# Performance work log

Measured on AMD Instinct MI355X. Metric: run time of the kernel, lower is better.

Reference implementation:

```python
import jax, jax.numpy as jnp
import numpy as np

HEAD_SIZE = 64

def setup_inputs() -> dict:
    key = jax.random.key(0)
    k1, k2, k3 = jax.random.split(key, 3)
    B, T, C = 4, 4096, 1024
    x = jax.random.normal(k1, (B, T, C), dtype=jnp.float32)
    # nn.Linear(C, head_size, bias=False); stored as [in, out] so x @ W matches x @ weight.T
    Wk = jax.random.normal(k2, (C, HEAD_SIZE), dtype=jnp.float32) * (C ** -0.5)
    Wv = jax.random.normal(k3, (C, HEAD_SIZE), dtype=jnp.float32) * (C ** -0.5)
    return {"x": x, "Wk": Wk, "Wv": Wv}

def reference(x, Wk, Wv):
    # Faithful to source: q = self.key(x)  (query projection is unused -> Q == K)
    B, T, C = x.shape
    k = jnp.einsum('btc,ch->bth', x, Wk)           # [B,T,H]
    q = jnp.einsum('btc,ch->bth', x, Wk)           # same projection (source bug)
    scores = jnp.einsum('bth,bsh->bts', q, k) * (HEAD_SIZE ** -0.5)  # [B,T,T]
    causal = jnp.tril(jnp.ones((T, T), dtype=bool))
    scores = jnp.where(causal, scores, -jnp.inf)
    weights = jax.nn.softmax(scores, axis=-1)      # dropout p=0 (eval) -> identity
    v = jnp.einsum('btc,ch->bth', x, Wv)
    out = jnp.einsum('bts,bsh->bth', weights, v)   # [B,T,H]
    return out
```

## Files before the change

### kernel.cpp

```cpp
#include <hip/hip_runtime.h>

typedef short bf16x8 __attribute__((ext_vector_type(8)));
typedef float f32x4 __attribute__((ext_vector_type(4)));
typedef float f32x16 __attribute__((ext_vector_type(16)));
typedef unsigned u32x4v __attribute__((ext_vector_type(4)));

#define T_SEQ 4096
#define CDIM  1024
#define HD    64
#define NROWS 16384

__device__ inline float exp2fast(float x) {
  return __builtin_amdgcn_exp2f(x);
}

__device__ inline unsigned short f2bf(float f) {
  unsigned u = __builtin_bit_cast(unsigned, f);
  u = (u + 0x7fffu + ((u >> 16) & 1u)) >> 16;
  return (unsigned short)u;
}
__device__ inline unsigned cvt_pk_bf16(float lo, float hi) {
  unsigned r;
  asm("v_cvt_pk_bf16_f32 %0, %1, %2" : "=v"(r) : "v"(lo), "v"(hi));
  return r;
}
__device__ inline float bf2f(unsigned short u) {
  unsigned v = (unsigned)u << 16;
  return __builtin_bit_cast(float, v);
}
__device__ inline void gload_lds16(const unsigned short* g, unsigned char* l) {
  __builtin_amdgcn_global_load_lds(
      (const __attribute__((address_space(1))) unsigned int*)(const void*)g,
      (__attribute__((address_space(3))) unsigned int*)(void*)l, 16, 0, 0);
}

__global__ __launch_bounds__(256) void prep_w(
    const float* __restrict__ Wk, const float* __restrict__ Wv,
    unsigned short* __restrict__ Wt) {
  __shared__ float tile[64][68];
  const int t = threadIdx.x;
  const int mat = blockIdx.x & 1;
  const int k0 = (blockIdx.x >> 1) * 64;
  const float* W = mat ? Wv : Wk;
  #pragma unroll
  for (int pp = 0; pp < 4; ++pp) {
    int idx = t + 256 * pp, row = idx >> 4, c4 = idx & 15;
    float4 v = *(const float4*)&W[(size_t)(k0 + row) * HD + c4 * 4];
    *(float4*)&tile[row][c4 * 4] = v;
  }
  __syncthreads();
  #pragma unroll
  for (int j = 0; j < 2; ++j) {
    int n = t & 63, j8 = (t >> 6) + 4 * j;
    unsigned ow[4];
    #pragma unroll
    for (int w = 0; w < 4; ++w)
      ow[w] = cvt_pk_bf16(tile[j8 * 8 + 2 * w][n], tile[j8 * 8 + 2 * w + 1][n]);
    u32x4v ov = {ow[0], ow[1], ow[2], ow[3]};
    *(u32x4v*)&Wt[(size_t)(mat * 64 + n) * CDIM + k0 + j8 * 8] = ov;
  }
}

__global__ __launch_bounds__(256) void proj_mfma(
    const float* __restrict__ x, const unsigned short* __restrict__ Wt,
    unsigned short* __restrict__ Kb, unsigned short* __restrict__ Vb) {
  __shared__ __align__(16) unsigned char xsb[16384];
  __shared__ __align__(16) unsigned char wsb[65536];
  const int tid = threadIdx.x;
  const int lane = tid & 63, wave = tid >> 6;
  const int wm = wave & 1, wn = wave >> 1;
  const int lg = lane >> 4, lc = lane & 15;
  const int row0 = blockIdx.x * 64;

  float4 xreg[8];
  auto load_x = [&](int kk) {
    #pragma unroll
    for (int p = 0; p < 8; ++p) {
      int idx = tid + 256 * p, r = idx >> 5, c4 = idx & 31;
      xreg[p] = *(const float4*)&x[(size_t)(row0 + r) * CDIM + kk + c4 * 4];
    }
  };
  auto write_x = [&]() {
    #pragma unroll
    for (int p = 0; p < 8; ++p) {
      int idx = tid + 256 * p, r = idx >> 5, c4 = idx & 31;
      uint2 v;
      v.x = cvt_pk_bf16(xreg[p].x, xreg[p].y);
      v.y = cvt_pk_bf16(xreg[p].z, xreg[p].w);
      int byt = (r * 256 + c4 * 8) ^ ((r & 7) << 4);
      *(uint2*)(xsb + byt) = v;
    }
  };
  auto gload_W = [&](int kk, int buf) {
    unsigned char* wb = wsb + buf * 32768;
    #pragma unroll
    for (int p = 0; p < 8; ++p) {
      int ci = p * 256 + tid;
      int r = ci >> 4;
      int c8 = (ci & 15) ^ (r & 7);
      gload_lds16(&Wt[(size_t)r * CDIM + kk + c8 * 8],
                  wb + (p * 256 + wave * 64) * 16);
    }
  };

  f32x4 acc[2][4];
  #pragma unroll
  for (int mf = 0; mf < 2; ++mf)
    #pragma unroll
    for (int nf = 0; nf < 4; ++nf) acc[mf][nf] = (f32x4){0.f, 0.f, 0.f, 0.f};

  gload_W(0, 0);
  load_x(0);
  for (int kk = 0; kk < CDIM; kk += 128) {
    const int cur = (kk >> 7) & 1;
    __syncthreads();
    write_x();
    __syncthreads();
    if (kk + 128 < CDIM) { gload_W(kk + 128, cur ^ 1); load_x(kk + 128); }
    const unsigned char* wb = wsb + cur * 32768;
    #pragma unroll
    for (int dd = 0; dd < 4; ++dd) {
      bf16x8 a[2], bfr[4];
      #pragma unroll
      for (int mf = 0; mf < 2; ++mf) {
        int r = wm * 32 + mf * 16 + lc;
        int sw = (r & 7) << 4;
        a[mf] = *(const bf16x8*)(xsb + ((r * 256 + dd * 64 + lg * 16) ^ sw));
      }
      #pragma unroll
      for (int nf = 0; nf < 4; ++nf) {
        int r = wn * 64 + nf * 16 + lc;
        int sw = (r & 7) << 4;
        bfr[nf] = *(const bf16x8*)(wb + ((r * 256 + dd * 64 + lg * 16) ^ sw));
      }
      __builtin_amdgcn_s_setprio(1);
      #pragma unroll
      for (int mf = 0; mf < 2; ++mf)
        #pragma unroll
        for (int nf = 0; nf < 4; ++nf)
          acc[mf][nf] = __builtin_amdgcn_mfma_f32_16x16x32_bf16(a[mf], bfr[nf], acc[mf][nf], 0, 0, 0);
      __builtin_amdgcn_s_setprio(0);
    }
  }

  unsigned short* Ob = (wn == 0) ? Kb : Vb;
  #pragma unroll
  for (int mf = 0; mf < 2; ++mf)
    #pragma unroll
    for (int r = 0; r < 4; ++r) {
      int rg = row0 + wm * 32 + mf * 16 + lg * 4 + r;
      #pragma unroll
      for (int nf = 0; nf < 4; ++nf)
        Ob[(size_t)rg * HD + nf * 16 + lc] = f2bf(acc[mf][nf][r]);
    }
}

__global__ __launch_bounds__(256) void attn_part(
    const unsigned short* __restrict__ Kb, const unsigned short* __restrict__ Vb,
    unsigned short* __restrict__ Opart, float* __restrict__ Ml) {
  __shared__ __align__(16) unsigned char lds[32768];

  const int tid = threadIdx.x;
  const int lane = tid & 63;
  const int wq = tid >> 6;
  const int hi = lane >> 5;
  const int lq = lane & 31;

  const int b = blockIdx.x & 3;
  int qb = 0, c = 0;
  {
    int u = blockIdx.x >> 2, acc = 0;
    for (int q = 31; q >= 0; --q) {
      int nch = (q + 2) >> 1;
      if (u < acc + nch) { qb = q; c = u - acc; break; }
      acc += nch;
    }
  }
  const int kstart = c * 256;
  const int kend = min(kstart + 256, (qb + 1) * 128);
  const int nit = (kend - kstart) >> 6;
  const int q0g = qb * 128 + wq * 32;
  const int qg = q0g + lq;
  const size_t base = (size_t)b * T_SEQ;
  const float SCALE2 = 0.18033688011112042f;

  bf16x8 qf[4];
  {
    const unsigned short* qp = &Kb[(base + q0g + lq) * HD];
    #pragma unroll
    for (int dd = 0; dd < 4; ++dd) {
      bf16x8 t = *(const bf16x8*)&qp[dd * 16 + hi * 8];
      const unsigned short* ts = (const unsigned short*)&t;
      unsigned ow[4];
      #pragma unroll
      for (int w = 0; w < 4; ++w)
        ow[w] = cvt_pk_bf16(bf2f(ts[2 * w]) * SCALE2, bf2f(ts[2 * w + 1]) * SCALE2);
      u32x4v ov = {ow[0], ow[1], ow[2], ow[3]};
      qf[dd] = __builtin_bit_cast(bf16x8, ov);
    }
  }

  f32x16 oT0, oT1;
  #pragma unroll
  for (int r = 0; r < 16; ++r) { oT0[r] = 0.f; oT1[r] = 0.f; }
  float mreg = -1e30f, lreg = 0.f;

  uint4 vreg0, vreg1;
  auto gload_K = [&](int jj, int buf) {
    const size_t kv0 = (base + kstart + (size_t)jj * 64) * HD;
    unsigned char* kb = lds + buf * 16384;
    #pragma unroll
    for (int p = 0; p < 2; ++p) {
      int ci = p * 256 + tid;
      int r = ci >> 3;
      int c8 = (ci & 7) ^ (r & 7);
      gload_lds16(&Kb[kv0 + (size_t)r * HD + c8 * 8],
                  kb + (p * 256 + (tid >> 6) * 64) * 16);
    }
  };
  auto load_v = [&](int jj) {
    const size_t kv0 = (base + kstart + (size_t)jj * 64) * HD;
    int key0 = (tid & 31) * 2, d0 = (tid >> 5) * 8;
    vreg0 = *(const uint4*)&Vb[kv0 + (size_t)key0 * HD + d0];
    vreg1 = *(const uint4*)&Vb[kv0 + (size_t)(key0 + 1) * HD + d0];
  };
  auto write_v = [&](int buf) {
    unsigned char* vb = lds + buf * 16384 + 8192;
    int key0 = (tid & 31) * 2, d0 = (tid >> 5) * 8;
    const unsigned short* pa = (const unsigned short*)&vreg0;
    const unsigned short* pb = (const unsigned short*)&vreg1;
    #pragma unroll
    for (int j = 0; j < 8; ++j) {
      unsigned val = (unsigned)pa[j] | ((unsigned)pb[j] << 16);
      int d = d0 + j;
      int byt = (d * 128 + key0 * 2) ^ ((d & 7) << 4);
      *(unsigned*)(vb + byt) = val;
    }
  };

  auto qk = [&](int buf, int ksub) -> f32x16 {
    const unsigned char* kb = lds + buf * 16384;
    f32x16 sacc;
    #pragma unroll
    for (int r = 0; r < 16; ++r) sacc[r] = 0.f;
    const int krow = ksub * 32 + lq;
    const int ksw = (krow & 7) << 4;
    #pragma unroll
    for (int dd = 0; dd < 4; ++dd) {
      bf16x8 kf = *(const bf16x8*)(kb + ((krow * 128 + dd * 32 + hi * 16) ^ ksw));
      sacc = __builtin_amdgcn_mfma_f32_32x32x16_bf16(kf, qf[dd], sacc, 0, 0, 0);
    }
    return sacc;
  };
  auto maskdiag = [&](f32x16& s, int kbase_s) {
    #pragma unroll
    for (int r = 0; r < 16; ++r) {
      int key = kbase_s + (r & 3) + 8 * (r >> 2) + 4 * hi;
      if (key > qg) s[r] = -1e38f;
    }
  };
  auto max16 = [&](const f32x16& s) -> float {
    return fmaxf(
        fmaxf(fmaxf(fmaxf(s[0], s[1]), fmaxf(s[2], s[3])),
              fmaxf(fmaxf(s[4], s[5]), fmaxf(s[6], s[7]))),
        fmaxf(fmaxf(fmaxf(s[8], s[9]), fmaxf(s[10], s[11])),
              fmaxf(fmaxf(s[12], s[13]), fmaxf(s[14], s[15]))));
  };
  auto pack2 = [&](const f32x16& s, bf16x8& p1, bf16x8& p2) {
    unsigned pk[8];
    #pragma unroll
    for (int i = 0; i < 8; ++i) pk[i] = cvt_pk_bf16(s[2 * i], s[2 * i + 1]);
    unsigned wA[4], wB[4];
    #pragma unroll
    for (int i = 0; i < 2; ++i) {
      unsigned a0 = pk[i], b0 = pk[2 + i];
      unsigned sa = (unsigned)__shfl_xor((int)a0, 32);
      unsigned sb = (unsigned)__shfl_xor((int)b0, 32);
      wA[i] = hi ? sb : a0;
      wA[2 + i] = hi ? b0 : sa;
      unsigned c0 = pk[4 + i], d0v = pk[6 + i];
      unsigned sc = (unsigned)__shfl_xor((int)c0, 32);
      unsigned sd = (unsigned)__shfl_xor((int)d0v, 32);
      wB[i] = hi ? sd : c0;
      wB[2 + i] = hi ? d0v : sc;
    }
    u32x4v t1v = {wA[0], wA[1], wA[2], wA[3]};
    u32x4v t2v = {wB[0], wB[1], wB[2], wB[3]};
    p1 = __builtin_bit_cast(bf16x8, t1v);
    p2 = __builtin_bit_cast(bf16x8, t2v);
  };
  auto pv = [&](int buf, int ksub, bf16x8 pb1, bf16x8 pb2) {
    const unsigned char* vb = lds + buf * 16384 + 8192;
    const int cb = ksub * 64;
    {
      int drow = lq;
      int swz = (drow & 7) << 4;
      bf16x8 v0 = *(const bf16x8*)(vb + ((drow * 128 + cb + hi * 16) ^ swz));
      bf16x8 v1 = *(const bf16x8*)(vb + ((drow * 128 + cb + 32 + hi * 16) ^ swz));
      oT0 = __builtin_amdgcn_mfma_f32_32x32x16_bf16(v0, pb1, oT0, 0, 0, 0);
      oT0 = __builtin_amdgcn_mfma_f32_32x32x16_bf16(v1, pb2, oT0, 0, 0, 0);
    }
    {
      int drow = 32 + lq;
      int swz = (drow & 7) << 4;
      bf16x8 v0 = *(const bf16x8*)(vb + ((drow * 128 + cb + hi * 16) ^ swz));
      bf16x8 v1 = *(const bf16x8*)(vb + ((drow * 128 + cb + 32 + hi * 16) ^ swz));
      oT1 = __builtin_amdgcn_mfma_f32_32x32x16_bf16(v0, pb1, oT1, 0, 0, 0);
      oT1 = __builtin_amdgcn_mfma_f32_32x32x16_bf16(v1, pb2, oT1, 0, 0, 0);
    }
  };

  gload_K(0, 0);
  load_v(0);
  write_v(0);
  for (int jj = 0; jj < nit; ++jj) {
    const int cur = jj & 1;
    __syncthreads();
    if (jj + 1 < nit) { gload_K(jj + 1, cur ^ 1); load_v(jj + 1); }
    const int kb0 = kstart + jj * 64;

    if (kb0 + 32 <= q0g) {
      __builtin_amdgcn_s_setprio(1);
      f32x16 s0 = qk(cur, 0);
      f32x16 s1 = qk(cur, 1);
      __builtin_amdgcn_s_setprio(0);
      if (kb0 + 32 == q0g) maskdiag(s1, kb0 + 32);
      float mx = fmaxf(max16(s0), max16(s1));
      mx = fmaxf(mx, __shfl_xor(mx, 32));
      if (!__all(mx <= mreg + 11.5f)) {
        float mn = fmaxf(mreg, mx);
        float al = exp2fast(mreg - mn);
        lreg *= al;
        #pragma unroll
        for (int r = 0; r < 16; ++r) { oT0[r] *= al; oT1[r] *= al; }
        mreg = mn;
      }
      float ps = 0.f;
      #pragma unroll
      for (int r = 0; r < 16; ++r) {
        float p0 = exp2fast(s0[r] - mreg);
        float p1 = exp2fast(s1[r] - mreg);
        ps += p0 + p1;
        s0[r] = p0;
        s1[r] = p1;
      }
      lreg += ps + __shfl_xor(ps, 32);
      bf16x8 pa1, pa2, pbb1, pbb2;
      pack2(s0, pa1, pa2);
      pack2(s1, pbb1, pbb2);
      __builtin_amdgcn_s_setprio(1);
      pv(cur, 0, pa1, pa2);
      pv(cur, 1, pbb1, pbb2);
      __builtin_amdgcn_s_setprio(0);
    } else if (kb0 <= q0g) {
      __builtin_amdgcn_s_setprio(1);
      f32x16 s0 = qk(cur, 0);
      __builtin_amdgcn_s_setprio(0);
      if (kb0 == q0g) maskdiag(s0, kb0);
      float mx = max16(s0);
      mx = fmaxf(mx, __shfl_xor(mx, 32));
      if (!__all(mx <= mreg + 11.5f)) {
        float mn = fmaxf(mreg, mx);
        float al = exp2fast(mreg - mn);
        lreg *= al;
        #pragma unroll
        for (int r = 0; r < 16; ++r) { oT0[r] *= al; oT1[r] *= al; }
        mreg = mn;
      }
      float ps = 0.f;
      #pragma unroll
      for (int r = 0; r < 16; ++r) {
        float p = exp2fast(s0[r] - mreg);
        ps += p;
        s0[r] = p;
      }
      lreg += ps + __shfl_xor(ps, 32);
      bf16x8 pa1, pa2;
      pack2(s0, pa1, pa2);
      __builtin_amdgcn_s_setprio(1);
      pv(cur, 0, pa1, pa2);
      __builtin_amdgcn_s_setprio(0);
    }

    if (jj + 1 < nit) write_v(cur ^ 1);
  }

  unsigned short* op = Opart + (size_t)blockIdx.x * 8192;
  const float invl = 1.0f / lreg;
  const int qrow = wq * 32 + lq;
  #pragma unroll
  for (int g = 0; g < 4; ++g) {
    int d0 = 8 * g + 4 * hi;
    uint2 w0, w1;
    w0.x = cvt_pk_bf16(oT0[4 * g] * invl, oT0[4 * g + 1] * invl);
    w0.y = cvt_pk_bf16(oT0[4 * g + 2] * invl, oT0[4 * g + 3] * invl);
    w1.x = cvt_pk_bf16(oT1[4 * g] * invl, oT1[4 * g + 1] * invl);
    w1.y = cvt_pk_bf16(oT1[4 * g + 2] * invl, oT1[4 * g + 3] * invl);
    *(uint2*)&op[qrow * 64 + d0] = w0;
    *(uint2*)&op[qrow * 64 + d0 + 32] = w1;
  }
  if (hi == 0) {
    Ml[(size_t)blockIdx.x * 256 + qrow * 2] = mreg;
    Ml[(size_t)blockIdx.x * 256 + qrow * 2 + 1] = lreg;
  }
}

__global__ __launch_bounds__(256) void attn_merge(
    const unsigned short* __restrict__ Opart, const float* __restrict__ Ml,
    float* __restrict__ out) {
  int g = blockIdx.x * 256 + threadIdx.x;
  int d8 = (g & 7) * 8;
  int q128 = (g >> 3) & 127;
  int qb = (g >> 10) & 31;
  int b = (g >> 15) & 3;
  int nch = (qb + 2) >> 1;
  int us = 0;
  for (int q = 31; q > qb; --q) us += (q + 2) >> 1;
  float M = -1e30f;
  for (int cc = 0; cc < nch; ++cc) {
    int part = (us + cc) * 4 + b;
    M = fmaxf(M, Ml[(size_t)part * 256 + q128 * 2]);
  }
  float L = 0.f;
  float o[8];
  #pragma unroll
  for (int j = 0; j < 8; ++j) o[j] = 0.f;
  for (int cc = 0; cc < nch; ++cc) {
    int part = (us + cc) * 4 + b;
    float mc = Ml[(size_t)part * 256 + q128 * 2];
    float lc = Ml[(size_t)part * 256 + q128 * 2 + 1];
    float w = exp2fast(mc - M) * lc;
    L += w;
    uint4 v = *(const uint4*)&Opart[(size_t)part * 8192 + q128 * 64 + d8];
    const unsigned short* pv = (const unsigned short*)&v;
    #pragma unroll
    for (int j = 0; j < 8; ++j) o[j] += w * bf2f(pv[j]);
  }
  float inv = 1.0f / L;
  size_t og = ((size_t)b * T_SEQ + qb * 128 + q128) * 64 + d8;
  float4 r0 = make_float4(o[0] * inv, o[1] * inv, o[2] * inv, o[3] * inv);
  float4 r1 = make_float4(o[4] * inv, o[5] * inv, o[6] * inv, o[7] * inv);
  *(float4*)&out[og] = r0;
  *(float4*)&out[og + 4] = r1;
}

extern "C" void kernel_launch(void* const* d_in, const int* in_sizes, int n_in,
                              void* d_out, int out_size, void* d_ws, size_t ws_size,
                              hipStream_t stream) {
  const float* x  = (const float*)d_in[0];
  const float* Wk = (const float*)d_in[1];
  const float* Wv = (const float*)d_in[2];
  unsigned short* Kb = (unsigned short*)d_ws;
  unsigned short* Vb = Kb + (size_t)NROWS * HD;
  unsigned short* Wt = Vb + (size_t)NROWS * HD;
  unsigned short* Opart = Wt + (size_t)128 * CDIM;
  float* Ml = (float*)(Opart + (size_t)1088 * 8192);
  float* o = (float*)d_out;

  prep_w<<<32, 256, 0, stream>>>(Wk, Wv, Wt);
  proj_mfma<<<256, 256, 0, stream>>>(x, Wt, Kb, Vb);
  attn_part<<<1088, 256, 0, stream>>>(Kb, Vb, Opart, Ml);
  attn_merge<<<512, 256, 0, stream>>>(Opart, Ml, o);
}
```

Before: 73.67 us.

## Enlarge attention query tile to 256 rows with 512-thread blocks

The partial-attention kernel now gives each block 256 query rows split across 8 waves (512 threads) instead of 128 rows across 4 waves. Each 256-key chunk always runs 4 iterations, so each K/V tile staged in LDS is reused by twice as many query rows. This halves the number of partial blocks and merge inputs. The trade-off is more waves sharing each barrier and fewer blocks for load balancing. Only half the threads load V, and diagonal chunks now do fully masked iterations for some waves.

```diff
diff --git a/kernel.cpp b/kernel.cpp
--- a/kernel.cpp
+++ b/kernel.cpp
@@ -155,7 +155,7 @@
     }
 }
 
-__global__ __launch_bounds__(256) void attn_part(
+__global__ __launch_bounds__(512) void attn_part(
     const unsigned short* __restrict__ Kb, const unsigned short* __restrict__ Vb,
     unsigned short* __restrict__ Opart, float* __restrict__ Ml) {
   __shared__ __align__(16) unsigned char lds[32768];
@@ -170,16 +170,14 @@
   int qb = 0, c = 0;
   {
     int u = blockIdx.x >> 2, acc = 0;
-    for (int q = 31; q >= 0; --q) {
-      int nch = (q + 2) >> 1;
+    for (int q = 15; q >= 0; --q) {
+      int nch = q + 1;
       if (u < acc + nch) { qb = q; c = u - acc; break; }
       acc += nch;
     }
   }
   const int kstart = c * 256;
-  const int kend = min(kstart + 256, (qb + 1) * 128);
-  const int nit = (kend - kstart) >> 6;
-  const int q0g = qb * 128 + wq * 32;
+  const int q0g = qb * 256 + wq * 32;
   const int qg = q0g + lq;
   const size_t base = (size_t)b * T_SEQ;
   const float SCALE2 = 0.18033688011112042f;
@@ -209,32 +207,31 @@
   auto gload_K = [&](int jj, int buf) {
     const size_t kv0 = (base + kstart + (size_t)jj * 64) * HD;
     unsigned char* kb = lds + buf * 16384;
-    #pragma unroll
-    for (int p = 0; p < 2; ++p) {
-      int ci = p * 256 + tid;
-      int r = ci >> 3;
-      int c8 = (ci & 7) ^ (r & 7);
-      gload_lds16(&Kb[kv0 + (size_t)r * HD + c8 * 8],
-                  kb + (p * 256 + (tid >> 6) * 64) * 16);
-    }
+    int r = tid >> 3;
+    int c8 = (tid & 7) ^ (r & 7);
+    gload_lds16(&Kb[kv0 + (size_t)r * HD + c8 * 8], kb + (tid >> 6) * 1024);
   };
   auto load_v = [&](int jj) {
-    const size_t kv0 = (base + kstart + (size_t)jj * 64) * HD;
-    int key0 = (tid & 31) * 2, d0 = (tid >> 5) * 8;
-    vreg0 = *(const uint4*)&Vb[kv0 + (size_t)key0 * HD + d0];
-    vreg1 = *(const uint4*)&Vb[kv0 + (size_t)(key0 + 1) * HD + d0];
+    if (tid < 256) {
+      const size_t kv0 = (base + kstart + (size_t)jj * 64) * HD;
+      int key0 = (tid & 31) * 2, d0 = (tid >> 5) * 8;
+      vreg0 = *(const uint4*)&Vb[kv0 + (size_t)key0 * HD + d0];
+      vreg1 = *(const uint4*)&Vb[kv0 + (size_t)(key0 + 1) * HD + d0];
+    }
   };
   auto write_v = [&](int buf) {
-    unsigned char* vb = lds + buf * 16384 + 8192;
-    int key0 = (tid & 31) * 2, d0 = (tid >> 5) * 8;
-    const unsigned short* pa = (const unsigned short*)&vreg0;
-    const unsigned short* pb = (const unsigned short*)&vreg1;
-    #pragma unroll
-    for (int j = 0; j < 8; ++j) {
-      unsigned val = (unsigned)pa[j] | ((unsigned)pb[j] << 16);
-      int d = d0 + j;
-      int byt = (d * 128 + key0 * 2) ^ ((d & 7) << 4);
-      *(unsigned*)(vb + byt) = val;
+    if (tid < 256) {
+      unsigned char* vb = lds + buf * 16384 + 8192;
+      int key0 = (tid & 31) * 2, d0 = (tid >> 5) * 8;
+      const unsigned short* pa = (const unsigned short*)&vreg0;
+      const unsigned short* pb = (const unsigned short*)&vreg1;
+      #pragma unroll
+      for (int j = 0; j < 8; ++j) {
+        unsigned val = (unsigned)pa[j] | ((unsigned)pb[j] << 16);
+        int d = d0 + j;
+        int byt = (d * 128 + key0 * 2) ^ ((d & 7) << 4);
+        *(unsigned*)(vb + byt) = val;
+      }
     }
   };
 
@@ -313,10 +310,10 @@
   gload_K(0, 0);
   load_v(0);
   write_v(0);
-  for (int jj = 0; jj < nit; ++jj) {
+  for (int jj = 0; jj < 4; ++jj) {
     const int cur = jj & 1;
     __syncthreads();
-    if (jj + 1 < nit) { gload_K(jj + 1, cur ^ 1); load_v(jj + 1); }
+    if (jj + 1 < 4) { gload_K(jj + 1, cur ^ 1); load_v(jj + 1); }
     const int kb0 = kstart + jj * 64;
 
     if (kb0 + 32 <= q0g) {
@@ -382,10 +379,11 @@
       __builtin_amdgcn_s_setprio(0);
     }
 
-    if (jj + 1 < nit) write_v(cur ^ 1);
-  }
-
-  unsigned short* op = Opart + (size_t)blockIdx.x * 8192;
+    if (jj + 1 < 4) write_v(cur ^ 1);
+  }
+
+  unsigned short* op = Opart + (size_t)blockIdx.x * 16384;
+  float* mlp = Ml + (size_t)blockIdx.x * 512;
   const float invl = 1.0f / lreg;
   const int qrow = wq * 32 + lq;
   #pragma unroll
@@ -400,8 +398,8 @@
     *(uint2*)&op[qrow * 64 + d0 + 32] = w1;
   }
   if (hi == 0) {
-    Ml[(size_t)blockIdx.x * 256 + qrow * 2] = mreg;
-    Ml[(size_t)blockIdx.x * 256 + qrow * 2 + 1] = lreg;
+    mlp[qrow * 2] = mreg;
+    mlp[qrow * 2 + 1] = lreg;
   }
 }
 
@@ -410,16 +408,18 @@
     float* __restrict__ out) {
   int g = blockIdx.x * 256 + threadIdx.x;
   int d8 = (g & 7) * 8;
-  int q128 = (g >> 3) & 127;
-  int qb = (g >> 10) & 31;
-  int b = (g >> 15) & 3;
-  int nch = (qb + 2) >> 1;
+  int row = g >> 3;
+  int b = row >> 12;
+  int t = row & (T_SEQ - 1);
+  int qp = t >> 8;
+  int r256 = t & 255;
+  int nch = qp + 1;
   int us = 0;
-  for (int q = 31; q > qb; --q) us += (q + 2) >> 1;
+  for (int q = 15; q > qp; --q) us += q + 1;
   float M = -1e30f;
   for (int cc = 0; cc < nch; ++cc) {
     int part = (us + cc) * 4 + b;
-    M = fmaxf(M, Ml[(size_t)part * 256 + q128 * 2]);
+    M = fmaxf(M, Ml[(size_t)part * 512 + r256 * 2]);
   }
   float L = 0.f;
   float o[8];
@@ -427,17 +427,17 @@
   for (int j = 0; j < 8; ++j) o[j] = 0.f;
   for (int cc = 0; cc < nch; ++cc) {
     int part = (us + cc) * 4 + b;
-    float mc = Ml[(size_t)part * 256 + q128 * 2];
-    float lc = Ml[(size_t)part * 256 + q128 * 2 + 1];
+    float mc = Ml[(size_t)part * 512 + r256 * 2];
+    float lc = Ml[(size_t)part * 512 + r256 * 2 + 1];
     float w = exp2fast(mc - M) * lc;
     L += w;
-    uint4 v = *(const uint4*)&Opart[(size_t)part * 8192 + q128 * 64 + d8];
+    uint4 v = *(const uint4*)&Opart[(size_t)part * 16384 + r256 * 64 + d8];
     const unsigned short* pv = (const unsigned short*)&v;
     #pragma unroll
     for (int j = 0; j < 8; ++j) o[j] += w * bf2f(pv[j]);
   }
   float inv = 1.0f / L;
-  size_t og = ((size_t)b * T_SEQ + qb * 128 + q128) * 64 + d8;
+  size_t og = ((size_t)b * T_SEQ + qp * 256 + r256) * 64 + d8;
   float4 r0 = make_float4(o[0] * inv, o[1] * inv, o[2] * inv, o[3] * inv);
   float4 r1 = make_float4(o[4] * inv, o[5] * inv, o[6] * inv, o[7] * inv);
   *(float4*)&out[og] = r0;
@@ -454,11 +454,11 @@
   unsigned short* Vb = Kb + (size_t)NROWS * HD;
   unsigned short* Wt = Vb + (size_t)NROWS * HD;
   unsigned short* Opart = Wt + (size_t)128 * CDIM;
-  float* Ml = (float*)(Opart + (size_t)1088 * 8192);
+  float* Ml = (float*)(Opart + (size_t)544 * 16384);
   float* o = (float*)d_out;
 
   prep_w<<<32, 256, 0, stream>>>(Wk, Wv, Wt);
   proj_mfma<<<256, 256, 0, stream>>>(x, Wt, Kb, Vb);
-  attn_part<<<1088, 256, 0, stream>>>(Kb, Vb, Opart, Ml);
+  attn_part<<<544, 512, 0, stream>>>(Kb, Vb, Opart, Ml);
   attn_merge<<<512, 256, 0, stream>>>(Opart, Ml, o);
 }
```

Result: faster. 71.79 us (-2.5%).
